# Kernel tuning notes

Measured on AMD Instinct MI355X. Metric: run time of the kernel, lower is better.

Reference implementation:

```python
import jax, jax.numpy as jnp
import numpy as np

Q, C, D, H, K, B, T = 10000, 200, 64, 64, 4, 512, 200
MAX_DISC = 10.0


def setup_inputs() -> dict:
    key = jax.random.key(0)
    ks = jax.random.split(key, 24)

    def p(k, shape, s=0.05):
        return jax.random.normal(k, shape, jnp.float32) * s

    mid_qd = (D + C) // 2   # 132
    mid_la = (H + C) // 2   # 132
    mid_dc = (D + 1) // 2   # 32
    inp = {
        'E_q': p(ks[0], (Q + 1, D)),
        'E_c': p(ks[1], (C + 1, D)),
        'E_it': p(ks[2], (101, D)),
        'E_ut': p(ks[3], (101, D)),
        'E_nh': p(ks[4], (101, D)),
        'W_fuse': p(ks[5], (D, 3 * D)), 'b_fuse': jnp.zeros((D,), jnp.float32),
        'W_ih': p(ks[6], (3 * H, 5 * D)), 'b_ih': jnp.zeros((3 * H,), jnp.float32),
        'W_hh': p(ks[7], (3 * H, H)), 'b_hh': jnp.zeros((3 * H,), jnp.float32),
        'qd_W1': p(ks[8], (mid_qd, D)), 'qd_b1': jnp.zeros((mid_qd,), jnp.float32),
        'qd_W2': p(ks[9], (C, mid_qd)), 'qd_b2': jnp.zeros((C,), jnp.float32),
        'la_W1': p(ks[10], (mid_la, H)), 'la_b1': jnp.zeros((mid_la,), jnp.float32),
        'la_W2': p(ks[11], (C, mid_la)), 'la_b2': jnp.zeros((C,), jnp.float32),
        'dc_W1': p(ks[12], (mid_dc, D)), 'dc_b1': jnp.zeros((mid_dc,), jnp.float32),
        'dc_W2': p(ks[13], (1, mid_dc)), 'dc_b2': jnp.zeros((1,), jnp.float32),
    }
    inp['question_seq'] = jax.random.randint(ks[14], (B, T), 0, Q + 1, jnp.int32)
    inp['correct_seq'] = jax.random.randint(ks[15], (B, T), 0, 2, jnp.int32)
    inp['interval_time_seq'] = jax.random.randint(ks[16], (B, T), 0, 101, jnp.int32)
    inp['use_time_seq'] = jax.random.randint(ks[17], (B, T), 0, 101, jnp.int32)
    inp['num_hint_seq'] = jax.random.randint(ks[18], (B, T), 0, 101, jnp.int32)
    inp['num_attempt_seq'] = jax.random.randint(ks[19], (B, T), 0, 101, jnp.int32)
    # per-question concept lists + padding mask (first nc entries valid)
    q2c = jax.random.randint(ks[20], (Q + 1, K), 0, C, jnp.int32)
    nc = jax.random.randint(ks[21], (Q + 1,), 1, K + 1, jnp.int32)
    mask = (jnp.arange(K, dtype=jnp.int32)[None, :] < nc[:, None]).astype(jnp.int32)
    inp['q2c_table'] = q2c
    inp['q2c_mask'] = mask
    rows = jnp.arange(Q + 1)[:, None]
    inp['Q_table'] = jnp.zeros((Q + 1, C), jnp.float32).at[rows, q2c].max(mask.astype(jnp.float32))
    return inp


def mlp2(x, W1, b1, W2, b2):
    # MLP4Proj, num_layer=2, eval-mode dropout == identity
    return jax.nn.relu(x @ W1.T + b1) @ W2.T + b2


def gru(x, W_ih, b_ih, W_hh, b_hh):
    # torch nn.GRU, 1 layer, batch_first; gate order r,z,n
    xp = jnp.einsum('btd,gd->btg', x, W_ih) + b_ih  # [B,T,3H]

    def step(h, xp_t):
        gh = h @ W_hh.T + b_hh
        xr, xz, xn = jnp.split(xp_t, 3, axis=-1)
        hr, hz, hn = jnp.split(gh, 3, axis=-1)
        r = jax.nn.sigmoid(xr + hr)
        z = jax.nn.sigmoid(xz + hz)
        n = jnp.tanh(xn + r * hn)
        h_new = (1.0 - z) * n + z * h
        return h_new, h_new

    h0 = jnp.zeros((x.shape[0], W_hh.shape[1]), x.dtype)
    _, hs = jax.lax.scan(step, h0, jnp.swapaxes(xp, 0, 1))
    return jnp.swapaxes(hs, 0, 1)  # [B,T,H]


def reference(E_q, E_c, E_it, E_ut, E_nh, W_fuse, b_fuse, W_ih, b_ih, W_hh, b_hh,
              qd_W1, qd_b1, qd_W2, qd_b2, la_W1, la_b1, la_W2, la_b2,
              dc_W1, dc_b1, dc_W2, dc_b2, Q_table,
              question_seq, correct_seq, interval_time_seq, use_time_seq,
              num_hint_seq, num_attempt_seq, q2c_table, q2c_mask):
    qe = E_q[question_seq]                                   # [B,T,D]
    # get_concept_emb: difficulty-weighted concept fusion
    qd = jax.nn.sigmoid(mlp2(qe, qd_W1, qd_b1, qd_W2, qd_b2))  # [B,T,C]
    qc_idx = q2c_table[question_seq]                          # [B,T,K]
    msk = q2c_mask[question_seq].astype(qe.dtype)             # [B,T,K]
    rel = jnp.take_along_axis(qd, qc_idx, axis=2) * msk       # [B,T,K]
    srel = rel.sum(-1, keepdims=True) + 1e-6
    ce = (rel[..., None] * E_c[qc_idx]).sum(-2) / srel        # [B,T,D]
    corr = jnp.broadcast_to(correct_seq[..., None].astype(qe.dtype), qe.shape)
    inter = jnp.concatenate([qe, ce, corr], axis=-1)          # [B,T,3D]
    # aux-info fusion (source bug: num_attempt also uses embed_num_hint)
    ut_nh_na = jnp.concatenate([E_ut[use_time_seq], E_nh[num_hint_seq], E_nh[num_attempt_seq]], axis=-1)
    fuse = ut_nh_na @ W_fuse.T + b_fuse                       # [B,T,D]
    x = jnp.concatenate([inter, E_it[interval_time_seq], fuse], axis=-1)  # [B,T,5D]
    latent = gru(x, W_ih, b_ih, W_hh, b_hh)                   # [B,T,H]
    # predict_score on shifted slices
    lat, qe2, qs2 = latent[:, :-1], qe[:, 1:], question_seq[:, 1:]
    ua = jax.nn.sigmoid(mlp2(lat, la_W1, la_b1, la_W2, la_b2))       # [B,T-1,C]
    disc = jax.nn.sigmoid(mlp2(qe2, dc_W1, dc_b1, dc_W2, dc_b2)) * MAX_DISC  # [B,T-1,1]
    qd2 = jax.nn.sigmoid(mlp2(qe2, qd_W1, qd_b1, qd_W2, qd_b2))      # [B,T-1,C]
    Qt = Q_table[qs2]                                                # [B,T-1,C]
    ua_m = ua * Qt
    qd_m = qd2 * Qt
    sw = qd_m.sum(-1, keepdims=True) + 1e-6
    y = disc * (ua_m - qd_m) / sw
    return jax.nn.sigmoid(y.sum(-1))                                 # [B,T-1]
```

## Files before the change

### kernel.cpp

```cpp
#include <hip/hip_runtime.h>
#include <hip/hip_fp16.h>

constexpr int QN  = 10001;
constexpr int BB  = 512;
constexpr int TT  = 200;
constexpr int QPB = 32;

__device__ __forceinline__ float sigm(float x) { return 1.f / (1.f + __expf(-x)); }
__device__ __forceinline__ float tanh_fast(float x) { return 1.f - 2.f / (1.f + __expf(2.f * x)); }

__device__ __forceinline__ unsigned packh_rtne(float lo, float hi) {
    return ((unsigned)__half_as_ushort(__float2half(hi)) << 16) |
            (unsigned)__half_as_ushort(__float2half(lo));
}

typedef _Float16 half2_t __attribute__((ext_vector_type(2)));
typedef float f4v __attribute__((ext_vector_type(4)));
__device__ __forceinline__ half2_t u2h(unsigned u) {
    union { unsigned u; half2_t h; } x; x.u = u; return x.h;
}

#if __has_builtin(__builtin_amdgcn_fdot2)
__device__ __forceinline__ float fdot2u(unsigned wu, unsigned hu, float acc) {
    return __builtin_amdgcn_fdot2(u2h(wu), u2h(hu), acc, false);
}
#else
__device__ __forceinline__ float fdot2u(unsigned wu, unsigned hu, float acc) {
    float wlo = __half2float(__ushort_as_half((unsigned short)(wu & 0xffffu)));
    float whi = __half2float(__ushort_as_half((unsigned short)(wu >> 16)));
    float hlo = __half2float(__ushort_as_half((unsigned short)(hu & 0xffffu)));
    float hhi = __half2float(__ushort_as_half((unsigned short)(hu >> 16)));
    return acc + wlo * hlo + whi * hhi;
}
#endif

typedef const __attribute__((address_space(1))) void cgv_t;
typedef __attribute__((address_space(3))) void lv_t;
__device__ __forceinline__ void glds16(const float* g, float* l) {
    __builtin_amdgcn_global_load_lds((cgv_t*)g, (lv_t*)l, 16, 0, 0);
}

__global__ void k_tables(const float* __restrict__ E_c, const float* __restrict__ E_it,
                         const float* __restrict__ E_ut, const float* __restrict__ E_nh,
                         const float* __restrict__ W_fuse, const float* __restrict__ b_fuse,
                         const float* __restrict__ W_ih, const float* __restrict__ b_ih,
                         float* __restrict__ T_c, float* __restrict__ T_it,
                         float* __restrict__ T_ut, float* __restrict__ T_nh, float* __restrict__ T_na,
                         float* __restrict__ bias0, float* __restrict__ Vcorr)
{
    int blk = blockIdx.x, j = threadIdx.x;
    __shared__ float s_e[64];
    __shared__ float s_t[64];
    const int ilv4 = (j & 63) * 4 + (j >> 6);

    if (blk < 201) {
        if (j < 64) s_e[j] = E_c[blk * 64 + j];
        __syncthreads();
        float a = 0.f;
        #pragma unroll
        for (int k = 0; k < 64; k++) a += W_ih[j * 320 + 64 + k] * s_e[k];
        T_c[blk * 192 + j] = a;
    } else if (blk < 302) {
        int r = blk - 201;
        if (j < 64) s_e[j] = E_it[r * 64 + j];
        __syncthreads();
        float a = 0.f;
        #pragma unroll
        for (int k = 0; k < 64; k++) a += W_ih[j * 320 + 192 + k] * s_e[k];
        T_it[r * 256 + ilv4] = a;
    } else if (blk < 605) {
        int which = (blk - 302) / 101;
        int r     = (blk - 302) % 101;
        const float* E = (which == 0) ? E_ut : E_nh;
        int fofs = which * 64;
        if (j < 64) s_e[j] = E[r * 64 + j];
        __syncthreads();
        if (j < 64) {
            float a = 0.f;
            #pragma unroll
            for (int d = 0; d < 64; d++) a += W_fuse[j * 192 + fofs + d] * s_e[d];
            s_t[j] = a;
        }
        __syncthreads();
        float a = 0.f;
        #pragma unroll
        for (int e = 0; e < 64; e++) a += W_ih[j * 320 + 256 + e] * s_t[e];
        float* outp = (which == 0) ? T_ut : ((which == 1) ? T_nh : T_na);
        outp[r * 256 + ilv4] = a;
    } else {
        float a = b_ih[j];
        #pragma unroll
        for (int e = 0; e < 64; e++) a += W_ih[j * 320 + 256 + e] * b_fuse[e];
        bias0[j] = a;
        float v = 0.f;
        #pragma unroll
        for (int k = 0; k < 64; k++) v += W_ih[j * 320 + 128 + k];
        Vcorr[j] = v;
    }
}

__global__ void __launch_bounds__(192) k_perq(
    const float* __restrict__ E_q, const float* __restrict__ W_ih,
    const float* __restrict__ qd_W1, const float* __restrict__ qd_b1,
    const float* __restrict__ qd_W2, const float* __restrict__ qd_b2,
    const float* __restrict__ dc_W1, const float* __restrict__ dc_b1,
    const float* __restrict__ dc_W2, const float* __restrict__ dc_b2,
    const int* __restrict__ q2c, const int* __restrict__ q2cm,
    const float* __restrict__ T_c,
    float* __restrict__ Xq, float* __restrict__ disc,
    float* __restrict__ qds, float* __restrict__ wdk)
{
    __shared__ float s_wbuf[192 * 66];
    __shared__ float s_qe[QPB][64];
    __shared__ float s_wq[QPB][4];
    __shared__ int   s_cq[QPB][4];
    __shared__ float s_hidw[3][136];

    const int tid = threadIdx.x, w = tid >> 6, l = tid & 63;
    const int q0 = blockIdx.x * QPB;

    for (int i = tid; i < 132 * 64; i += 192)
        s_wbuf[(i >> 6) * 66 + (i & 63)] = qd_W1[i];
    for (int i = tid; i < 32 * 64; i += 192)
        s_wbuf[(132 + (i >> 6)) * 66 + (i & 63)] = dc_W1[i];
    for (int i = tid; i < QPB * 64; i += 192) {
        int qq = i >> 6, q = q0 + qq;
        s_qe[qq][i & 63] = E_q[(q < QN ? q : 0) * 64 + (i & 63)];
    }
    __syncthreads();

    for (int qq = w; qq < QPB; qq += 3) {
        int q = q0 + qq;
        bool valid = q < QN;
        int qc = valid ? q : 0;
        int cc[4], mm[4];
        #pragma unroll
        for (int k = 0; k < 4; k++) { cc[k] = q2c[qc * 4 + k]; mm[k] = q2cm[qc * 4 + k]; }

        float qe[64];
        #pragma unroll
        for (int k4 = 0; k4 < 16; k4++) {
            float4 v = *(const float4*)(&s_qe[qq][k4 * 4]);
            qe[4 * k4] = v.x; qe[4 * k4 + 1] = v.y; qe[4 * k4 + 2] = v.z; qe[4 * k4 + 3] = v.w;
        }

        auto rowdot = [&](int r) {
            const float* wr = s_wbuf + r * 66;
            float a = 0.f;
            #pragma unroll
            for (int jj = 0; jj < 32; jj++) {
                float2 ww = *(const float2*)(wr + 2 * jj);
                a += ww.x * qe[2 * jj] + ww.y * qe[2 * jj + 1];
            }
            return a;
        };

        s_hidw[w][l]      = fmaxf(rowdot(l)      + qd_b1[l],      0.f);
        s_hidw[w][64 + l] = fmaxf(rowdot(64 + l) + qd_b1[64 + l], 0.f);
        if (l < 4)
            s_hidw[w][128 + l] = fmaxf(rowdot(128 + l) + qd_b1[128 + l], 0.f);
        float dch = 0.f;
        if (l < 32) dch = fmaxf(rowdot(132 + l) + dc_b1[l], 0.f);

        int g = l >> 4, li = l & 15;
        int c = cc[g];
        float acc = 0.f;
        #pragma unroll
        for (int i = 0; i < 9; i++) {
            int m = li + 16 * i;
            if (m < 132) acc += qd_W2[c * 132 + m] * s_hidw[w][m];
        }
        acc += __shfl_xor(acc, 1); acc += __shfl_xor(acc, 2);
        acc += __shfl_xor(acc, 4); acc += __shfl_xor(acc, 8);
        float r0 = __shfl(acc, 0), r1 = __shfl(acc, 16);
        float r2 = __shfl(acc, 32), r3 = __shfl(acc, 48);

        float raw[4] = { sigm(r0 + qd_b2[cc[0]]), sigm(r1 + qd_b2[cc[1]]),
                         sigm(r2 + qd_b2[cc[2]]), sigm(r3 + qd_b2[cc[3]]) };
        float rel[4];
        #pragma unroll
        for (int k = 0; k < 4; k++) rel[k] = raw[k] * (float)mm[k];
        float sr = rel[0] + rel[1] + rel[2] + rel[3] + 1e-6f;

        float qsum = 0.f, wdv[4];
        #pragma unroll
        for (int k = 0; k < 4; k++) {
            float wd = 0.f;
            if (mm[k]) {
                bool dup = false;
                for (int jj = 0; jj < k; jj++)
                    if (mm[jj] && cc[jj] == cc[k]) dup = true;
                if (!dup) { wd = 1.f; qsum += raw[k]; }
            }
            wdv[k] = wd;
        }
        if (l < 4) { s_wq[qq][l] = rel[l] / sr; s_cq[qq][l] = cc[l]; }
        if (valid) {
            if (l < 4) wdk[q * 4 + l] = wdv[l];
            if (l == 0) qds[q] = qsum;
        }

        float dv = (l < 32) ? dch * dc_W2[l] : 0.f;
        dv += __shfl_xor(dv, 1);  dv += __shfl_xor(dv, 2);
        dv += __shfl_xor(dv, 4);  dv += __shfl_xor(dv, 8);
        dv += __shfl_xor(dv, 16);
        if (valid && l == 0) disc[q] = sigm(dv + dc_b2[0]) * 10.f;
    }

    __syncthreads();
    for (int i = tid; i < 192 * 64; i += 192) {
        int r = i >> 6, k = i & 63;
        s_wbuf[r * 66 + k] = W_ih[r * 320 + k];
    }
    __syncthreads();

    for (int qq = w; qq < QPB; qq += 3) {
        int q = q0 + qq;
        if (q >= QN) continue;

        float qe[64];
        #pragma unroll
        for (int k4 = 0; k4 < 16; k4++) {
            float4 v = *(const float4*)(&s_qe[qq][k4 * 4]);
            qe[4 * k4] = v.x; qe[4 * k4 + 1] = v.y; qe[4 * k4 + 2] = v.z; qe[4 * k4 + 3] = v.w;
        }
        float wq[4]; int cq[4];
        #pragma unroll
        for (int k = 0; k < 4; k++) { wq[k] = s_wq[qq][k]; cq[k] = s_cq[qq][k]; }

        #pragma unroll
        for (int rr = 0; rr < 3; rr++) {
            int row = rr * 64 + l;
            const float* wr = s_wbuf + row * 66;
            float a = 0.f;
            #pragma unroll
            for (int jj = 0; jj < 32; jj++) {
                float2 ww = *(const float2*)(wr + 2 * jj);
                a += ww.x * qe[2 * jj] + ww.y * qe[2 * jj + 1];
            }
            #pragma unroll
            for (int k = 0; k < 4; k++) a += wq[k] * T_c[cq[k] * 192 + row];
            Xq[q * 256 + l * 4 + rr] = a;
        }
    }
}

__global__ void
__launch_bounds__(64)
__attribute__((amdgpu_waves_per_eu(1, 1)))
k_gru(
    const float* __restrict__ W_hh, const float* __restrict__ b_hh,
    const float* __restrict__ XqI, const float* __restrict__ TitI, const float* __restrict__ TutI,
    const float* __restrict__ TnhI, const float* __restrict__ TnaI,
    const float* __restrict__ b0, const float* __restrict__ vc,
    const int* __restrict__ qseq, const int* __restrict__ cseq, const int* __restrict__ itseq,
    const int* __restrict__ utseq, const int* __restrict__ nhseq, const int* __restrict__ naseq,
    float* __restrict__ latent)
{
    const int j = threadIdx.x, b = blockIdx.x;
    const int j4 = 4 * j;

    __shared__ float s_gb[4][5][64][4];
    __shared__ unsigned s_hp[32];
    __shared__ int s_ix[6 * TT];

    const int base = b * TT;
    for (int i = j; i < TT; i += 64) {
        s_ix[i]          = qseq[base + i];
        s_ix[TT + i]     = cseq[base + i];
        s_ix[2 * TT + i] = itseq[base + i];
        s_ix[3 * TT + i] = utseq[base + i];
        s_ix[4 * TT + i] = nhseq[base + i];
        s_ix[5 * TT + i] = naseq[base + i];
    }

    unsigned wr[32], wz[32], wn[32];
    {
        const float4* p0 = (const float4*)(W_hh + j * 64);
        const float4* p1 = (const float4*)(W_hh + (64 + j) * 64);
        const float4* p2 = (const float4*)(W_hh + (128 + j) * 64);
        #pragma unroll
        for (int k = 0; k < 16; k++) {
            float4 a = p0[k], bq = p1[k], c = p2[k];
            wr[2 * k] = packh_rtne(a.x, a.y);  wr[2 * k + 1] = packh_rtne(a.z, a.w);
            wz[2 * k] = packh_rtne(bq.x, bq.y); wz[2 * k + 1] = packh_rtne(bq.z, bq.w);
            wn[2 * k] = packh_rtne(c.x, c.y);  wn[2 * k + 1] = packh_rtne(c.z, c.w);
        }
    }
    #pragma unroll
    for (int k = 0; k < 32; k++)
        asm volatile("" : "+v"(wr[k]), "+v"(wz[k]), "+v"(wn[k]));

    const float bhr = b_hh[j], bhz = b_hh[64 + j], bhn = b_hh[128 + j];
    const float b0r = b0[j],   b0z = b0[64 + j],   b0n = b0[128 + j];
    const float vcr = vc[j],   vcz = vc[64 + j],   vcn = vc[128 + j];

    if (j < 32) s_hp[j] = 0u;
    float hj = 0.f;

    float cA, cB, cC, cD;

#define GISSUE(S, CCV, tt) { \
        int q_ = s_ix[tt], c_ = s_ix[TT + tt], it_ = s_ix[2 * TT + tt]; \
        int ut_ = s_ix[3 * TT + tt], nh_ = s_ix[4 * TT + tt], na_ = s_ix[5 * TT + tt]; \
        CCV = (float)c_; \
        glds16(XqI  + q_  * 256 + j4, &s_gb[S][0][0][0]); \
        glds16(TitI + it_ * 256 + j4, &s_gb[S][1][0][0]); \
        glds16(TutI + ut_ * 256 + j4, &s_gb[S][2][0][0]); \
        glds16(TnhI + nh_ * 256 + j4, &s_gb[S][3][0][0]); \
        glds16(TnaI + na_ * 256 + j4, &s_gb[S][4][0][0]); \
    }

#define STEP(S, CCV, tcur, WN, REF) { \
        asm volatile("s_waitcnt vmcnt(" WN ")" ::: "memory"); \
        f4v g0 = *(const f4v*)&s_gb[S][0][j][0]; \
        f4v g1 = *(const f4v*)&s_gb[S][1][j][0]; \
        f4v g2 = *(const f4v*)&s_gb[S][2][j][0]; \
        f4v g3 = *(const f4v*)&s_gb[S][3][j][0]; \
        f4v g4 = *(const f4v*)&s_gb[S][4][j][0]; \
        asm volatile("s_waitcnt lgkmcnt(0)" ::: "memory"); \
        float xr = b0r + CCV * vcr + (((g0.x + g1.x) + (g2.x + g3.x)) + g4.x); \
        float xz = b0z + CCV * vcz + (((g0.y + g1.y) + (g2.y + g3.y)) + g4.y); \
        float xn = b0n + CCV * vcn + (((g0.z + g1.z) + (g2.z + g3.z)) + g4.z); \
        if (REF) GISSUE(S, CCV, (tcur) + 4); \
        float ar0 = 0.f, ar1 = 0.f, ar2 = 0.f, ar3 = 0.f; \
        float az0 = 0.f, az1 = 0.f, az2 = 0.f, az3 = 0.f; \
        float an0 = 0.f, an1 = 0.f, an2 = 0.f, an3 = 0.f; \
        const uint4* hp4 = (const uint4*)s_hp; \
        _Pragma("unroll") \
        for (int k4 = 0; k4 < 8; k4++) { \
            uint4 hh = hp4[k4]; \
            ar0 = fdot2u(wr[4 * k4 + 0], hh.x, ar0); \
            ar1 = fdot2u(wr[4 * k4 + 1], hh.y, ar1); \
            ar2 = fdot2u(wr[4 * k4 + 2], hh.z, ar2); \
            ar3 = fdot2u(wr[4 * k4 + 3], hh.w, ar3); \
            az0 = fdot2u(wz[4 * k4 + 0], hh.x, az0); \
            az1 = fdot2u(wz[4 * k4 + 1], hh.y, az1); \
            az2 = fdot2u(wz[4 * k4 + 2], hh.z, az2); \
            az3 = fdot2u(wz[4 * k4 + 3], hh.w, az3); \
            an0 = fdot2u(wn[4 * k4 + 0], hh.x, an0); \
            an1 = fdot2u(wn[4 * k4 + 1], hh.y, an1); \
            an2 = fdot2u(wn[4 * k4 + 2], hh.z, an2); \
            an3 = fdot2u(wn[4 * k4 + 3], hh.w, an3); \
        } \
        float ar = ((ar0 + ar1) + (ar2 + ar3)) + bhr; \
        float az = ((az0 + az1) + (az2 + az3)) + bhz; \
        float an = ((an0 + an1) + (an2 + an3)) + bhn; \
        float r = sigm(xr + ar); \
        float z = sigm(xz + az); \
        float n = tanh_fast(xn + r * an); \
        hj = (1.f - z) * n + z * hj; \
        latent[(size_t)(base + (tcur)) * 64 + j] = hj; \
        float hnb = __shfl_xor(hj, 1); \
        unsigned pk = (j & 1) ? packh_rtne(hnb, hj) : packh_rtne(hj, hnb); \
        if (!(j & 1)) s_hp[j >> 1] = pk; \
    }

    GISSUE(0, cA, 0);
    GISSUE(1, cB, 1);
    GISSUE(2, cC, 2);
    GISSUE(3, cD, 3);

    STEP(0, cA, 0, "15", 1);
    STEP(1, cB, 1, "16", 1);
    STEP(2, cC, 2, "17", 1);
    STEP(3, cD, 3, "18", 1);

    for (int t = 4; t <= TT - 8; t += 4) {
        STEP(0, cA, t,     "18", 1);
        STEP(1, cB, t + 1, "18", 1);
        STEP(2, cC, t + 2, "18", 1);
        STEP(3, cD, t + 3, "18", 1);
    }
    STEP(0, cA, TT - 4, "18", 0);
    STEP(1, cB, TT - 3, "12", 0);
    STEP(2, cC, TT - 2, "6",  0);
    STEP(3, cD, TT - 1, "0",  0);
#undef STEP
#undef GISSUE
}

__global__ void __launch_bounds__(256) k_final(
    const float* __restrict__ latent, const int* __restrict__ qseq,
    const float* __restrict__ la_W1, const float* __restrict__ la_b1,
    const float* __restrict__ la_W2, const float* __restrict__ la_b2,
    const int* __restrict__ q2c,
    const float* __restrict__ disc, const float* __restrict__ qds,
    const float* __restrict__ wdk, float* __restrict__ out)
{
    __shared__ unsigned short s_w2[200 * 132];
    __shared__ float s_b2[200];

    const int tid = threadIdx.x;
    for (int i = tid; i < 200 * 132; i += 256)
        s_w2[i] = __half_as_ushort(__float2half(la_W2[i]));
    for (int i = tid; i < 200; i += 256) s_b2[i] = la_b2[i];
    __syncthreads();

    int o = blockIdx.x * blockDim.x + tid;
    if (o >= BB * (TT - 1)) return;
    int b = o / (TT - 1), t = o - b * (TT - 1);

    const float* lat = latent + (size_t)(b * TT + t) * 64;
    float l[64];
    #pragma unroll
    for (int k4 = 0; k4 < 16; k4++) {
        float4 v = ((const float4*)lat)[k4];
        l[k4 * 4] = v.x; l[k4 * 4 + 1] = v.y; l[k4 * 4 + 2] = v.z; l[k4 * 4 + 3] = v.w;
    }

    int q = qseq[b * TT + t + 1];
    int c0 = q2c[q * 4], c1 = q2c[q * 4 + 1], c2 = q2c[q * 4 + 2], c3 = q2c[q * 4 + 3];
    const unsigned short* w0p = s_w2 + c0 * 132;
    const unsigned short* w1p = s_w2 + c1 * 132;
    const unsigned short* w2p = s_w2 + c2 * 132;
    const unsigned short* w3p = s_w2 + c3 * 132;

    float u0 = 0.f, u1 = 0.f, u2 = 0.f, u3 = 0.f;
    for (int m = 0; m < 132; m++) {
        float a = la_b1[m];
        const float* w = la_W1 + m * 64;
        #pragma unroll
        for (int k = 0; k < 64; k++) a += w[k] * l[k];
        float hm = fmaxf(a, 0.f);
        u0 += __half2float(__ushort_as_half(w0p[m])) * hm;
        u1 += __half2float(__ushort_as_half(w1p[m])) * hm;
        u2 += __half2float(__ushort_as_half(w2p[m])) * hm;
        u3 += __half2float(__ushort_as_half(w3p[m])) * hm;
    }

    float w0 = wdk[q * 4], w1 = wdk[q * 4 + 1], w2 = wdk[q * 4 + 2], w3 = wdk[q * 4 + 3];
    float us = w0 * sigm(u0 + s_b2[c0]) + w1 * sigm(u1 + s_b2[c1])
             + w2 * sigm(u2 + s_b2[c2]) + w3 * sigm(u3 + s_b2[c3]);
    float qs = qds[q];
    float y = disc[q] * (us - qs) / (qs + 1e-6f);
    out[o] = sigm(y);
}

extern "C" void kernel_launch(void* const* d_in, const int* in_sizes, int n_in,
                              void* d_out, int out_size, void* d_ws, size_t ws_size,
                              hipStream_t stream)
{
    const float* E_q    = (const float*)d_in[0];
    const float* E_c    = (const float*)d_in[1];
    const float* E_it   = (const float*)d_in[2];
    const float* E_ut   = (const float*)d_in[3];
    const float* E_nh   = (const float*)d_in[4];
    const float* W_fuse = (const float*)d_in[5];
    const float* b_fuse = (const float*)d_in[6];
    const float* W_ih   = (const float*)d_in[7];
    const float* b_ih   = (const float*)d_in[8];
    const float* W_hh   = (const float*)d_in[9];
    const float* b_hh   = (const float*)d_in[10];
    const float* qd_W1  = (const float*)d_in[11];
    const float* qd_b1  = (const float*)d_in[12];
    const float* qd_W2  = (const float*)d_in[13];
    const float* qd_b2  = (const float*)d_in[14];
    const float* la_W1  = (const float*)d_in[15];
    const float* la_b1  = (const float*)d_in[16];
    const float* la_W2  = (const float*)d_in[17];
    const float* la_b2  = (const float*)d_in[18];
    const float* dc_W1  = (const float*)d_in[19];
    const float* dc_b1  = (const float*)d_in[20];
    const float* dc_W2  = (const float*)d_in[21];
    const float* dc_b2  = (const float*)d_in[22];

    int off = (in_sizes[23] == QN * 200) ? 1 : 0;
    const int* qseq  = (const int*)d_in[23 + off];
    const int* cseq  = (const int*)d_in[24 + off];
    const int* itseq = (const int*)d_in[25 + off];
    const int* utseq = (const int*)d_in[26 + off];
    const int* nhseq = (const int*)d_in[27 + off];
    const int* naseq = (const int*)d_in[28 + off];
    const int* q2c   = (const int*)d_in[29 + off];
    const int* q2cm  = (const int*)d_in[30 + off];

    float* ws = (float*)d_ws;
    size_t o = 0;
    float* T_c  = ws + o; o += (size_t)201 * 192;
    float* Tit  = ws + o; o += (size_t)101 * 256;
    float* Tut  = ws + o; o += (size_t)101 * 256;
    float* Tnh  = ws + o; o += (size_t)101 * 256;
    float* Tna  = ws + o; o += (size_t)101 * 256;
    float* b0   = ws + o; o += 192;
    float* vc   = ws + o; o += 192;
    float* Xq   = ws + o; o += (size_t)QN * 256;
    float* disc = ws + o; o += QN;
    float* qds  = ws + o; o += QN;
    float* wdk  = ws + o; o += (size_t)QN * 4;
    float* latent = ws + o; o += (size_t)BB * TT * 64;

    float* outp = (float*)d_out;

    k_tables<<<606, 192, 0, stream>>>(E_c, E_it, E_ut, E_nh, W_fuse, b_fuse, W_ih, b_ih,
                                      T_c, Tit, Tut, Tnh, Tna, b0, vc);
    k_perq<<<(QN + QPB - 1) / QPB, 192, 0, stream>>>(E_q, W_ih, qd_W1, qd_b1, qd_W2, qd_b2,
                                                     dc_W1, dc_b1, dc_W2, dc_b2, q2c, q2cm, T_c,
                                                     Xq, disc, qds, wdk);
    k_gru<<<BB, 64, 0, stream>>>(W_hh, b_hh, Xq, Tit, Tut, Tnh, Tna, b0, vc,
                                 qseq, cseq, itseq, utseq, nhseq, naseq, latent);
    k_final<<<(BB * (TT - 1) + 255) / 256, 256, 0, stream>>>(latent, qseq, la_W1, la_b1,
                                                             la_W2, la_b2, q2c, disc, qds, wdk, outp);
}
```

Measured before the change: 328.4 us.

## Interleave two independent GRU sequences per wave to hide recurrence latency

```diff
diff --git a/kernel.cpp b/kernel.cpp
--- a/kernel.cpp
+++ b/kernel.cpp
@@ -257,21 +257,22 @@
     const int* __restrict__ utseq, const int* __restrict__ nhseq, const int* __restrict__ naseq,
     float* __restrict__ latent)
 {
-    const int j = threadIdx.x, b = blockIdx.x;
+    const int j = threadIdx.x, b2 = blockIdx.x;
     const int j4 = 4 * j;
 
-    __shared__ float s_gb[4][5][64][4];
-    __shared__ unsigned s_hp[32];
-    __shared__ int s_ix[6 * TT];
-
-    const int base = b * TT;
+    __shared__ float s_gb[2][2][5][64][4];
+    __shared__ unsigned s_hp[2][32];
+    __shared__ int s_ix[2][6][TT];
+
+    const int base0 = (2 * b2) * TT;
+    const int base1 = base0 + TT;
     for (int i = j; i < TT; i += 64) {
-        s_ix[i]          = qseq[base + i];
-        s_ix[TT + i]     = cseq[base + i];
-        s_ix[2 * TT + i] = itseq[base + i];
-        s_ix[3 * TT + i] = utseq[base + i];
-        s_ix[4 * TT + i] = nhseq[base + i];
-        s_ix[5 * TT + i] = naseq[base + i];
+        s_ix[0][0][i] = qseq[base0 + i];  s_ix[1][0][i] = qseq[base1 + i];
+        s_ix[0][1][i] = cseq[base0 + i];  s_ix[1][1][i] = cseq[base1 + i];
+        s_ix[0][2][i] = itseq[base0 + i]; s_ix[1][2][i] = itseq[base1 + i];
+        s_ix[0][3][i] = utseq[base0 + i]; s_ix[1][3][i] = utseq[base1 + i];
+        s_ix[0][4][i] = nhseq[base0 + i]; s_ix[1][4][i] = nhseq[base1 + i];
+        s_ix[0][5][i] = naseq[base0 + i]; s_ix[1][5][i] = naseq[base1 + i];
     }
 
     unsigned wr[32], wz[32], wn[32];
@@ -295,38 +296,41 @@
     const float b0r = b0[j],   b0z = b0[64 + j],   b0n = b0[128 + j];
     const float vcr = vc[j],   vcz = vc[64 + j],   vcn = vc[128 + j];
 
-    if (j < 32) s_hp[j] = 0u;
-    float hj = 0.f;
-
-    float cA, cB, cC, cD;
-
-#define GISSUE(S, CCV, tt) { \
-        int q_ = s_ix[tt], c_ = s_ix[TT + tt], it_ = s_ix[2 * TT + tt]; \
-        int ut_ = s_ix[3 * TT + tt], nh_ = s_ix[4 * TT + tt], na_ = s_ix[5 * TT + tt]; \
+    if (j < 32) { s_hp[0][j] = 0u; s_hp[1][j] = 0u; }
+    float hjA = 0.f, hjB = 0.f;
+
+    float cA0, cA1, cB0, cB1;
+
+#define GISSUE(SA, SL, CCV, tt) { \
+        int q_ = s_ix[SA][0][tt], c_ = s_ix[SA][1][tt], it_ = s_ix[SA][2][tt]; \
+        int ut_ = s_ix[SA][3][tt], nh_ = s_ix[SA][4][tt], na_ = s_ix[SA][5][tt]; \
         CCV = (float)c_; \
-        glds16(XqI  + q_  * 256 + j4, &s_gb[S][0][0][0]); \
-        glds16(TitI + it_ * 256 + j4, &s_gb[S][1][0][0]); \
-        glds16(TutI + ut_ * 256 + j4, &s_gb[S][2][0][0]); \
-        glds16(TnhI + nh_ * 256 + j4, &s_gb[S][3][0][0]); \
-        glds16(TnaI + na_ * 256 + j4, &s_gb[S][4][0][0]); \
-    }
-
-#define STEP(S, CCV, tcur, WN, REF) { \
+        glds16(XqI  + q_  * 256 + j4, &s_gb[SA][SL][0][0][0]); \
+        glds16(TitI + it_ * 256 + j4, &s_gb[SA][SL][1][0][0]); \
+        glds16(TutI + ut_ * 256 + j4, &s_gb[SA][SL][2][0][0]); \
+        glds16(TnhI + nh_ * 256 + j4, &s_gb[SA][SL][3][0][0]); \
+        glds16(TnaI + na_ * 256 + j4, &s_gb[SA][SL][4][0][0]); \
+    }
+
+#define LPH(SA, SL, CCV, tt, WN, REF, XR, XZ, XN) { \
         asm volatile("s_waitcnt vmcnt(" WN ")" ::: "memory"); \
-        f4v g0 = *(const f4v*)&s_gb[S][0][j][0]; \
-        f4v g1 = *(const f4v*)&s_gb[S][1][j][0]; \
-        f4v g2 = *(const f4v*)&s_gb[S][2][j][0]; \
-        f4v g3 = *(const f4v*)&s_gb[S][3][j][0]; \
-        f4v g4 = *(const f4v*)&s_gb[S][4][j][0]; \
+        f4v g0 = *(const f4v*)&s_gb[SA][SL][0][j][0]; \
+        f4v g1 = *(const f4v*)&s_gb[SA][SL][1][j][0]; \
+        f4v g2 = *(const f4v*)&s_gb[SA][SL][2][j][0]; \
+        f4v g3 = *(const f4v*)&s_gb[SA][SL][3][j][0]; \
+        f4v g4 = *(const f4v*)&s_gb[SA][SL][4][j][0]; \
         asm volatile("s_waitcnt lgkmcnt(0)" ::: "memory"); \
-        float xr = b0r + CCV * vcr + (((g0.x + g1.x) + (g2.x + g3.x)) + g4.x); \
-        float xz = b0z + CCV * vcz + (((g0.y + g1.y) + (g2.y + g3.y)) + g4.y); \
-        float xn = b0n + CCV * vcn + (((g0.z + g1.z) + (g2.z + g3.z)) + g4.z); \
-        if (REF) GISSUE(S, CCV, (tcur) + 4); \
+        XR = b0r + CCV * vcr + (((g0.x + g1.x) + (g2.x + g3.x)) + g4.x); \
+        XZ = b0z + CCV * vcz + (((g0.y + g1.y) + (g2.y + g3.y)) + g4.y); \
+        XN = b0n + CCV * vcn + (((g0.z + g1.z) + (g2.z + g3.z)) + g4.z); \
+        if (REF) GISSUE(SA, SL, CCV, (tt) + 2); \
+    }
+
+#define DPH(SA, HJ, tcur, XR, XZ, XN) { \
         float ar0 = 0.f, ar1 = 0.f, ar2 = 0.f, ar3 = 0.f; \
         float az0 = 0.f, az1 = 0.f, az2 = 0.f, az3 = 0.f; \
         float an0 = 0.f, an1 = 0.f, an2 = 0.f, an3 = 0.f; \
-        const uint4* hp4 = (const uint4*)s_hp; \
+        const uint4* hp4 = (const uint4*)s_hp[SA]; \
         _Pragma("unroll") \
         for (int k4 = 0; k4 < 8; k4++) { \
             uint4 hh = hp4[k4]; \
@@ -346,37 +350,53 @@
         float ar = ((ar0 + ar1) + (ar2 + ar3)) + bhr; \
         float az = ((az0 + az1) + (az2 + az3)) + bhz; \
         float an = ((an0 + an1) + (an2 + an3)) + bhn; \
-        float r = sigm(xr + ar); \
-        float z = sigm(xz + az); \
-        float n = tanh_fast(xn + r * an); \
-        hj = (1.f - z) * n + z * hj; \
-        latent[(size_t)(base + (tcur)) * 64 + j] = hj; \
-        float hnb = __shfl_xor(hj, 1); \
-        unsigned pk = (j & 1) ? packh_rtne(hnb, hj) : packh_rtne(hj, hnb); \
-        if (!(j & 1)) s_hp[j >> 1] = pk; \
-    }
-
-    GISSUE(0, cA, 0);
-    GISSUE(1, cB, 1);
-    GISSUE(2, cC, 2);
-    GISSUE(3, cD, 3);
-
-    STEP(0, cA, 0, "15", 1);
-    STEP(1, cB, 1, "16", 1);
-    STEP(2, cC, 2, "17", 1);
-    STEP(3, cD, 3, "18", 1);
-
-    for (int t = 4; t <= TT - 8; t += 4) {
-        STEP(0, cA, t,     "18", 1);
-        STEP(1, cB, t + 1, "18", 1);
-        STEP(2, cC, t + 2, "18", 1);
-        STEP(3, cD, t + 3, "18", 1);
-    }
-    STEP(0, cA, TT - 4, "18", 0);
-    STEP(1, cB, TT - 3, "12", 0);
-    STEP(2, cC, TT - 2, "6",  0);
-    STEP(3, cD, TT - 1, "0",  0);
-#undef STEP
+        float r = sigm(XR + ar); \
+        float z = sigm(XZ + az); \
+        float n = tanh_fast(XN + r * an); \
+        HJ = (1.f - z) * n + z * HJ; \
+        latent[(size_t)(((SA) ? base1 : base0) + (tcur)) * 64 + j] = HJ; \
+        float hnb = __shfl_xor(HJ, 1); \
+        unsigned pk = (j & 1) ? packh_rtne(hnb, HJ) : packh_rtne(HJ, hnb); \
+        if (!(j & 1)) s_hp[SA][j >> 1] = pk; \
+    }
+
+    float xrA, xzA, xnA, xrB, xzB, xnB;
+
+    GISSUE(0, 0, cA0, 0);
+    GISSUE(1, 0, cB0, 0);
+    GISSUE(0, 1, cA1, 1);
+    GISSUE(1, 1, cB1, 1);
+
+    LPH(0, 0, cA0, 0, "15", 1, xrA, xzA, xnA);
+    LPH(1, 0, cB0, 0, "15", 1, xrB, xzB, xnB);
+    DPH(0, hjA, 0, xrA, xzA, xnA);
+    DPH(1, hjB, 0, xrB, xzB, xnB);
+    LPH(0, 1, cA1, 1, "16", 1, xrA, xzA, xnA);
+    LPH(1, 1, cB1, 1, "16", 1, xrB, xzB, xnB);
+    DPH(0, hjA, 1, xrA, xzA, xnA);
+    DPH(1, hjB, 1, xrB, xzB, xnB);
+
+    for (int t = 2; t <= TT - 4; t += 2) {
+        LPH(0, 0, cA0, t, "17", 1, xrA, xzA, xnA);
+        LPH(1, 0, cB0, t, "17", 1, xrB, xzB, xnB);
+        DPH(0, hjA, t, xrA, xzA, xnA);
+        DPH(1, hjB, t, xrB, xzB, xnB);
+        LPH(0, 1, cA1, t + 1, "17", 1, xrA, xzA, xnA);
+        LPH(1, 1, cB1, t + 1, "17", 1, xrB, xzB, xnB);
+        DPH(0, hjA, t + 1, xrA, xzA, xnA);
+        DPH(1, hjB, t + 1, xrB, xzB, xnB);
+    }
+
+    LPH(0, 0, cA0, TT - 2, "17", 0, xrA, xzA, xnA);
+    LPH(1, 0, cB0, TT - 2, "12", 0, xrB, xzB, xnB);
+    DPH(0, hjA, TT - 2, xrA, xzA, xnA);
+    DPH(1, hjB, TT - 2, xrB, xzB, xnB);
+    LPH(0, 1, cA1, TT - 1, "7", 0, xrA, xzA, xnA);
+    LPH(1, 1, cB1, TT - 1, "2", 0, xrB, xzB, xnB);
+    DPH(0, hjA, TT - 1, xrA, xzA, xnA);
+    DPH(1, hjB, TT - 1, xrB, xzB, xnB);
+#undef DPH
+#undef LPH
 #undef GISSUE
 }
 
@@ -497,8 +517,8 @@
     k_perq<<<(QN + QPB - 1) / QPB, 192, 0, stream>>>(E_q, W_ih, qd_W1, qd_b1, qd_W2, qd_b2,
                                                      dc_W1, dc_b1, dc_W2, dc_b2, q2c, q2cm, T_c,
                                                      Xq, disc, qds, wdk);
-    k_gru<<<BB, 64, 0, stream>>>(W_hh, b_hh, Xq, Tit, Tut, Tnh, Tna, b0, vc,
-                                 qseq, cseq, itseq, utseq, nhseq, naseq, latent);
+    k_gru<<<BB / 2, 64, 0, stream>>>(W_hh, b_hh, Xq, Tit, Tut, Tnh, Tna, b0, vc,
+                                     qseq, cseq, itseq, utseq, nhseq, naseq, latent);
     k_final<<<(BB * (TT - 1) + 255) / 256, 256, 0, stream>>>(latent, qseq, la_W1, la_b1,
                                                              la_W2, la_b2, q2c, disc, qds, wdk, outp);
 }
```

New measurement: 451.4 us. 37.4% more time.

## Fuse final scoring MLP into GRU kernel using LDS latent and fp16 dot2

Applied to the files above, without the earlier changes.

```diff
diff --git a/kernel.cpp b/kernel.cpp
--- a/kernel.cpp
+++ b/kernel.cpp
@@ -44,9 +44,11 @@
                          const float* __restrict__ E_ut, const float* __restrict__ E_nh,
                          const float* __restrict__ W_fuse, const float* __restrict__ b_fuse,
                          const float* __restrict__ W_ih, const float* __restrict__ b_ih,
+                         const float* __restrict__ la_W1, const float* __restrict__ la_W2,
                          float* __restrict__ T_c, float* __restrict__ T_it,
                          float* __restrict__ T_ut, float* __restrict__ T_nh, float* __restrict__ T_na,
-                         float* __restrict__ bias0, float* __restrict__ Vcorr)
+                         float* __restrict__ bias0, float* __restrict__ Vcorr,
+                         unsigned* __restrict__ w1h, unsigned* __restrict__ w2h)
 {
     int blk = blockIdx.x, j = threadIdx.x;
     __shared__ float s_e[64];
@@ -87,7 +89,7 @@
         for (int e = 0; e < 64; e++) a += W_ih[j * 320 + 256 + e] * s_t[e];
         float* outp = (which == 0) ? T_ut : ((which == 1) ? T_nh : T_na);
         outp[r * 256 + ilv4] = a;
-    } else {
+    } else if (blk == 605) {
         float a = b_ih[j];
         #pragma unroll
         for (int e = 0; e < 64; e++) a += W_ih[j * 320 + 256 + e] * b_fuse[e];
@@ -96,6 +98,16 @@
         #pragma unroll
         for (int k = 0; k < 64; k++) v += W_ih[j * 320 + 128 + k];
         Vcorr[j] = v;
+    } else if (blk < 628) {
+        int i = (blk - 606) * 192 + j;
+        int m = i >> 5, k = i & 31;
+        w1h[i] = packh_rtne(la_W1[m * 64 + 2 * k], la_W1[m * 64 + 2 * k + 1]);
+    } else {
+        int i = (blk - 628) * 192 + j;
+        if (i < 200 * 68) {
+            int c = i / 68, k = i - c * 68;
+            w2h[i] = (k < 66) ? packh_rtne(la_W2[c * 132 + 2 * k], la_W2[c * 132 + 2 * k + 1]) : 0u;
+        }
     }
 }
 
@@ -246,8 +258,7 @@
 }
 
 __global__ void
-__launch_bounds__(64)
-__attribute__((amdgpu_waves_per_eu(1, 1)))
+__launch_bounds__(256)
 k_gru(
     const float* __restrict__ W_hh, const float* __restrict__ b_hh,
     const float* __restrict__ XqI, const float* __restrict__ TitI, const float* __restrict__ TutI,
@@ -255,17 +266,23 @@
     const float* __restrict__ b0, const float* __restrict__ vc,
     const int* __restrict__ qseq, const int* __restrict__ cseq, const int* __restrict__ itseq,
     const int* __restrict__ utseq, const int* __restrict__ nhseq, const int* __restrict__ naseq,
-    float* __restrict__ latent)
+    const unsigned* __restrict__ w1h, const float* __restrict__ la_b1,
+    const unsigned* __restrict__ w2h, const float* __restrict__ la_b2,
+    const int* __restrict__ q2c,
+    const float* __restrict__ disc, const float* __restrict__ qds,
+    const float* __restrict__ wdk, float* __restrict__ out)
 {
-    const int j = threadIdx.x, b = blockIdx.x;
+    const int tid = threadIdx.x, b = blockIdx.x;
+    const int wave = tid >> 6, j = tid & 63;
     const int j4 = 4 * j;
 
     __shared__ float s_gb[4][5][64][4];
+    __shared__ int s_ix[6 * TT];
     __shared__ unsigned s_hp[32];
-    __shared__ int s_ix[6 * TT];
+    __shared__ float s_lat[TT][66];
 
     const int base = b * TT;
-    for (int i = j; i < TT; i += 64) {
+    for (int i = tid; i < TT; i += 256) {
         s_ix[i]          = qseq[base + i];
         s_ix[TT + i]     = cseq[base + i];
         s_ix[2 * TT + i] = itseq[base + i];
@@ -273,32 +290,33 @@
         s_ix[4 * TT + i] = nhseq[base + i];
         s_ix[5 * TT + i] = naseq[base + i];
     }
-
-    unsigned wr[32], wz[32], wn[32];
-    {
-        const float4* p0 = (const float4*)(W_hh + j * 64);
-        const float4* p1 = (const float4*)(W_hh + (64 + j) * 64);
-        const float4* p2 = (const float4*)(W_hh + (128 + j) * 64);
-        #pragma unroll
-        for (int k = 0; k < 16; k++) {
-            float4 a = p0[k], bq = p1[k], c = p2[k];
-            wr[2 * k] = packh_rtne(a.x, a.y);  wr[2 * k + 1] = packh_rtne(a.z, a.w);
-            wz[2 * k] = packh_rtne(bq.x, bq.y); wz[2 * k + 1] = packh_rtne(bq.z, bq.w);
-            wn[2 * k] = packh_rtne(c.x, c.y);  wn[2 * k + 1] = packh_rtne(c.z, c.w);
-        }
-    }
-    #pragma unroll
-    for (int k = 0; k < 32; k++)
-        asm volatile("" : "+v"(wr[k]), "+v"(wz[k]), "+v"(wn[k]));
-
-    const float bhr = b_hh[j], bhz = b_hh[64 + j], bhn = b_hh[128 + j];
-    const float b0r = b0[j],   b0z = b0[64 + j],   b0n = b0[128 + j];
-    const float vcr = vc[j],   vcz = vc[64 + j],   vcn = vc[128 + j];
-
-    if (j < 32) s_hp[j] = 0u;
-    float hj = 0.f;
-
-    float cA, cB, cC, cD;
+    if (tid < 32) s_hp[tid] = 0u;
+    __syncthreads();
+
+    if (wave == 0) {
+        unsigned wr[32], wz[32], wn[32];
+        {
+            const float4* p0 = (const float4*)(W_hh + j * 64);
+            const float4* p1 = (const float4*)(W_hh + (64 + j) * 64);
+            const float4* p2 = (const float4*)(W_hh + (128 + j) * 64);
+            #pragma unroll
+            for (int k = 0; k < 16; k++) {
+                float4 a = p0[k], bq = p1[k], c = p2[k];
+                wr[2 * k] = packh_rtne(a.x, a.y);  wr[2 * k + 1] = packh_rtne(a.z, a.w);
+                wz[2 * k] = packh_rtne(bq.x, bq.y); wz[2 * k + 1] = packh_rtne(bq.z, bq.w);
+                wn[2 * k] = packh_rtne(c.x, c.y);  wn[2 * k + 1] = packh_rtne(c.z, c.w);
+            }
+        }
+        #pragma unroll
+        for (int k = 0; k < 32; k++)
+            asm volatile("" : "+v"(wr[k]), "+v"(wz[k]), "+v"(wn[k]));
+
+        const float bhr = b_hh[j], bhz = b_hh[64 + j], bhn = b_hh[128 + j];
+        const float b0r = b0[j],   b0z = b0[64 + j],   b0n = b0[128 + j];
+        const float vcr = vc[j],   vcz = vc[64 + j],   vcn = vc[128 + j];
+
+        float hj = 0.f;
+        float cA, cB, cC, cD;
 
 #define GISSUE(S, CCV, tt) { \
         int q_ = s_ix[tt], c_ = s_ix[TT + tt], it_ = s_ix[2 * TT + tt]; \
@@ -350,91 +368,90 @@
         float z = sigm(xz + az); \
         float n = tanh_fast(xn + r * an); \
         hj = (1.f - z) * n + z * hj; \
-        latent[(size_t)(base + (tcur)) * 64 + j] = hj; \
+        s_lat[tcur][j] = hj; \
         float hnb = __shfl_xor(hj, 1); \
         unsigned pk = (j & 1) ? packh_rtne(hnb, hj) : packh_rtne(hj, hnb); \
         if (!(j & 1)) s_hp[j >> 1] = pk; \
     }
 
-    GISSUE(0, cA, 0);
-    GISSUE(1, cB, 1);
-    GISSUE(2, cC, 2);
-    GISSUE(3, cD, 3);
-
-    STEP(0, cA, 0, "15", 1);
-    STEP(1, cB, 1, "16", 1);
-    STEP(2, cC, 2, "17", 1);
-    STEP(3, cD, 3, "18", 1);
-
-    for (int t = 4; t <= TT - 8; t += 4) {
-        STEP(0, cA, t,     "18", 1);
-        STEP(1, cB, t + 1, "18", 1);
-        STEP(2, cC, t + 2, "18", 1);
-        STEP(3, cD, t + 3, "18", 1);
-    }
-    STEP(0, cA, TT - 4, "18", 0);
-    STEP(1, cB, TT - 3, "12", 0);
-    STEP(2, cC, TT - 2, "6",  0);
-    STEP(3, cD, TT - 1, "0",  0);
+        GISSUE(0, cA, 0);
+        GISSUE(1, cB, 1);
+        GISSUE(2, cC, 2);
+        GISSUE(3, cD, 3);
+
+        STEP(0, cA, 0, "15", 1);
+        STEP(1, cB, 1, "15", 1);
+        STEP(2, cC, 2, "15", 1);
+        STEP(3, cD, 3, "15", 1);
+
+        for (int t = 4; t <= TT - 8; t += 4) {
+            STEP(0, cA, t,     "15", 1);
+            STEP(1, cB, t + 1, "15", 1);
+            STEP(2, cC, t + 2, "15", 1);
+            STEP(3, cD, t + 3, "15", 1);
+        }
+        STEP(0, cA, TT - 4, "15", 0);
+        STEP(1, cB, TT - 3, "10", 0);
+        STEP(2, cC, TT - 2, "5",  0);
+        STEP(3, cD, TT - 1, "0",  0);
 #undef STEP
 #undef GISSUE
-}
-
-__global__ void __launch_bounds__(256) k_final(
-    const float* __restrict__ latent, const int* __restrict__ qseq,
-    const float* __restrict__ la_W1, const float* __restrict__ la_b1,
-    const float* __restrict__ la_W2, const float* __restrict__ la_b2,
-    const int* __restrict__ q2c,
-    const float* __restrict__ disc, const float* __restrict__ qds,
-    const float* __restrict__ wdk, float* __restrict__ out)
-{
-    __shared__ unsigned short s_w2[200 * 132];
-    __shared__ float s_b2[200];
-
-    const int tid = threadIdx.x;
-    for (int i = tid; i < 200 * 132; i += 256)
-        s_w2[i] = __half_as_ushort(__float2half(la_W2[i]));
-    for (int i = tid; i < 200; i += 256) s_b2[i] = la_b2[i];
+    }
     __syncthreads();
 
-    int o = blockIdx.x * blockDim.x + tid;
-    if (o >= BB * (TT - 1)) return;
-    int b = o / (TT - 1), t = o - b * (TT - 1);
-
-    const float* lat = latent + (size_t)(b * TT + t) * 64;
-    float l[64];
-    #pragma unroll
-    for (int k4 = 0; k4 < 16; k4++) {
-        float4 v = ((const float4*)lat)[k4];
-        l[k4 * 4] = v.x; l[k4 * 4 + 1] = v.y; l[k4 * 4 + 2] = v.z; l[k4 * 4 + 3] = v.w;
-    }
-
-    int q = qseq[b * TT + t + 1];
-    int c0 = q2c[q * 4], c1 = q2c[q * 4 + 1], c2 = q2c[q * 4 + 2], c3 = q2c[q * 4 + 3];
-    const unsigned short* w0p = s_w2 + c0 * 132;
-    const unsigned short* w1p = s_w2 + c1 * 132;
-    const unsigned short* w2p = s_w2 + c2 * 132;
-    const unsigned short* w3p = s_w2 + c3 * 132;
-
-    float u0 = 0.f, u1 = 0.f, u2 = 0.f, u3 = 0.f;
-    for (int m = 0; m < 132; m++) {
-        float a = la_b1[m];
-        const float* w = la_W1 + m * 64;
-        #pragma unroll
-        for (int k = 0; k < 64; k++) a += w[k] * l[k];
-        float hm = fmaxf(a, 0.f);
-        u0 += __half2float(__ushort_as_half(w0p[m])) * hm;
-        u1 += __half2float(__ushort_as_half(w1p[m])) * hm;
-        u2 += __half2float(__ushort_as_half(w2p[m])) * hm;
-        u3 += __half2float(__ushort_as_half(w3p[m])) * hm;
-    }
-
-    float w0 = wdk[q * 4], w1 = wdk[q * 4 + 1], w2 = wdk[q * 4 + 2], w3 = wdk[q * 4 + 3];
-    float us = w0 * sigm(u0 + s_b2[c0]) + w1 * sigm(u1 + s_b2[c1])
-             + w2 * sigm(u2 + s_b2[c2]) + w3 * sigm(u3 + s_b2[c3]);
-    float qs = qds[q];
-    float y = disc[q] * (us - qs) / (qs + 1e-6f);
-    out[o] = sigm(y);
+    if (tid < TT - 1) {
+        const int t = tid;
+        unsigned L[32];
+        {
+            const float4* lp = (const float4*)&s_lat[t][0];
+            #pragma unroll
+            for (int kk = 0; kk < 16; kk++) {
+                float4 v = lp[kk];
+                L[2 * kk]     = packh_rtne(v.x, v.y);
+                L[2 * kk + 1] = packh_rtne(v.z, v.w);
+            }
+        }
+
+        unsigned hidpk[66];
+        float hprev = 0.f;
+        #pragma unroll
+        for (int m = 0; m < 132; m++) {
+            const unsigned* w1r = w1h + m * 32;
+            float a0 = 0.f, a1 = 0.f, a2 = 0.f, a3 = 0.f;
+            #pragma unroll
+            for (int k = 0; k < 32; k += 4) {
+                a0 = fdot2u(w1r[k],     L[k],     a0);
+                a1 = fdot2u(w1r[k + 1], L[k + 1], a1);
+                a2 = fdot2u(w1r[k + 2], L[k + 2], a2);
+                a3 = fdot2u(w1r[k + 3], L[k + 3], a3);
+            }
+            float hm = fmaxf(((a0 + a1) + (a2 + a3)) + la_b1[m], 0.f);
+            if (m & 1) hidpk[m >> 1] = packh_rtne(hprev, hm);
+            else hprev = hm;
+        }
+
+        int q = s_ix[t + 1];
+        float u[4];
+        #pragma unroll
+        for (int kc = 0; kc < 4; kc++) {
+            int c = q2c[q * 4 + kc];
+            const unsigned* w2r = w2h + c * 68;
+            float u0 = 0.f, u1 = 0.f;
+            #pragma unroll
+            for (int k = 0; k < 66; k += 2) {
+                u0 = fdot2u(w2r[k],     hidpk[k],     u0);
+                u1 = fdot2u(w2r[k + 1], hidpk[k + 1], u1);
+            }
+            u[kc] = u0 + u1 + la_b2[c];
+        }
+
+        float us = 0.f;
+        #pragma unroll
+        for (int kc = 0; kc < 4; kc++) us += wdk[q * 4 + kc] * sigm(u[kc]);
+        float qs = qds[q];
+        float y = disc[q] * (us - qs) / (qs + 1e-6f);
+        out[(size_t)b * (TT - 1) + t] = sigm(y);
+    }
 }
 
 extern "C" void kernel_launch(void* const* d_in, const int* in_sizes, int n_in,
@@ -488,17 +505,18 @@
     float* disc = ws + o; o += QN;
     float* qds  = ws + o; o += QN;
     float* wdk  = ws + o; o += (size_t)QN * 4;
-    float* latent = ws + o; o += (size_t)BB * TT * 64;
+    unsigned* w1h = (unsigned*)(ws + o); o += (size_t)132 * 32;
+    unsigned* w2h = (unsigned*)(ws + o); o += (size_t)200 * 68;
 
     float* outp = (float*)d_out;
 
-    k_tables<<<606, 192, 0, stream>>>(E_c, E_it, E_ut, E_nh, W_fuse, b_fuse, W_ih, b_ih,
-                                      T_c, Tit, Tut, Tnh, Tna, b0, vc);
+    k_tables<<<699, 192, 0, stream>>>(E_c, E_it, E_ut, E_nh, W_fuse, b_fuse, W_ih, b_ih,
+                                      la_W1, la_W2,
+                                      T_c, Tit, Tut, Tnh, Tna, b0, vc, w1h, w2h);
     k_perq<<<(QN + QPB - 1) / QPB, 192, 0, stream>>>(E_q, W_ih, qd_W1, qd_b1, qd_W2, qd_b2,
                                                      dc_W1, dc_b1, dc_W2, dc_b2, q2c, q2cm, T_c,
                                                      Xq, disc, qds, wdk);
-    k_gru<<<BB, 64, 0, stream>>>(W_hh, b_hh, Xq, Tit, Tut, Tnh, Tna, b0, vc,
-                                 qseq, cseq, itseq, utseq, nhseq, naseq, latent);
-    k_final<<<(BB * (TT - 1) + 255) / 256, 256, 0, stream>>>(latent, qseq, la_W1, la_b1,
-                                                             la_W2, la_b2, q2c, disc, qds, wdk, outp);
-}
+    k_gru<<<BB, 256, 0, stream>>>(W_hh, b_hh, Xq, Tit, Tut, Tnh, Tna, b0, vc,
+                                  qseq, cseq, itseq, utseq, nhseq, naseq,
+                                  w1h, la_b1, w2h, la_b2, q2c, disc, qds, wdk, outp);
+}
```

Result: no change. 331.9 us (+1.1%).
